# Kernel tuning notes

Hardware: AMD Instinct MI355X
Metric: run time of the kernel (lower is better)

Reference implementation:

```python
import jax, jax.numpy as jnp
import numpy as np
from jax import lax
from jax.scipy.special import logsumexp

V, E, H, T = 30000, 512, 512, 76   # vocab, embed, hidden, num_tags
B, S = 256, 128
HD = H // 2                        # per-direction hidden


def setup_inputs() -> dict:
    key = jax.random.key(0)
    ks = jax.random.split(key, 18)
    n = lambda k, shp: jax.random.normal(k, shp, dtype=jnp.float32) * 0.05
    return {
        "input_ids": jax.random.randint(ks[0], (B, S), 0, V),
        "tag_ids":   jax.random.randint(ks[1], (B, S), 0, 74),
        "lengths":   jax.random.randint(ks[2], (B,), 1, S + 1),
        "embed_table": n(ks[3], (V, E)),
        "W_ih_f": n(ks[4], (4 * HD, E)),  "W_hh_f": n(ks[5], (4 * HD, HD)),
        "b_ih_f": n(ks[6], (4 * HD,)),    "b_hh_f": n(ks[7], (4 * HD,)),
        "W_ih_b": n(ks[8], (4 * HD, E)),  "W_hh_b": n(ks[9], (4 * HD, HD)),
        "b_ih_b": n(ks[10], (4 * HD,)),   "b_hh_b": n(ks[11], (4 * HD,)),
        "W_out": n(ks[12], (T, H)),       "b_out": n(ks[13], (T,)),
        "start_trans": n(ks[14], (T,)),   "end_trans": n(ks[15], (T,)),
        "trans": n(ks[16], (T, T)),
        "h0": jax.random.normal(ks[17], (2, B, HD), dtype=jnp.float32),
        "c0": jax.random.normal(jax.random.fold_in(key, 99), (2, B, HD), dtype=jnp.float32),
    }


def _run_lstm(x, h, c, Wih, Whh, b):
    # x: (S,B,E); PyTorch gate order i,f,g,o
    def step(carry, xt):
        h, c = carry
        z = xt @ Wih.T + h @ Whh.T + b
        i, f, g, o = jnp.split(z, 4, axis=-1)
        c = jax.nn.sigmoid(f) * c + jax.nn.sigmoid(i) * jnp.tanh(g)
        h = jax.nn.sigmoid(o) * jnp.tanh(c)
        return (h, c), h
    _, hs = lax.scan(step, (h, c), x)
    return hs  # (S,B,HD)


def _crf_nll(em, tags, mask, start_trans, end_trans, trans):
    # em: (S,B,T) emissions, tags: (S,B) int, mask: (S,B) bool, mask[0]=True
    nb = em.shape[1]
    bidx = jnp.arange(nb)
    # --- numerator: score of gold path ---
    score0 = start_trans[tags[0]] + em[0, bidx, tags[0]]
    def num_step(carry, inp):
        score, prev = carry
        em_t, tag_t, m_t = inp
        s = trans[prev, tag_t] + em_t[bidx, tag_t]
        score = score + jnp.where(m_t, s, jnp.zeros_like(s))
        prev = jnp.where(m_t, tag_t, prev)
        return (score, prev), None
    (score, last_tags), _ = lax.scan(num_step, (score0, tags[0]), (em[1:], tags[1:], mask[1:]))
    score = score + end_trans[last_tags]
    # --- denominator: log partition via forward algorithm ---
    alpha0 = start_trans[None, :] + em[0]  # (B,T)
    def den_step(alpha, inp):
        em_t, m_t = inp
        nxt = logsumexp(alpha[:, :, None] + trans[None, :, :] + em_t[:, None, :], axis=1)
        return jnp.where(m_t[:, None], nxt, alpha), None
    alpha, _ = lax.scan(den_step, alpha0, (em[1:], mask[1:]))
    logZ = logsumexp(alpha + end_trans[None, :], axis=1)
    return score - logZ  # (B,) log-likelihood


def reference(input_ids, tag_ids, lengths, embed_table,
              W_ih_f, W_hh_f, b_ih_f, b_hh_f,
              W_ih_b, W_hh_b, b_ih_b, b_hh_b,
              W_out, b_out, start_trans, end_trans, trans, h0, c0):
    s = input_ids.shape[1]
    mask = jnp.arange(s)[None, :] < lengths[:, None]   # (B,S) left-aligned, col 0 all True
    x = embed_table[input_ids].transpose(1, 0, 2)      # (S,B,E)
    hf = _run_lstm(x, h0[0], c0[0], W_ih_f, W_hh_f, b_ih_f + b_hh_f)
    hb = _run_lstm(x[::-1], h0[1], c0[1], W_ih_b, W_hh_b, b_ih_b + b_hh_b)[::-1]
    feats = jnp.concatenate([hf, hb], axis=-1)         # (S,B,H)
    em = feats @ W_out.T + b_out                       # (S,B,T)
    llh = _crf_nll(em, tag_ids.T, mask.T, start_trans, end_trans, trans)
    return -jnp.mean(llh)                              # reduction='mean', negated
```

## Files before the change

kernel.cpp:

```cpp
#include <hip/hip_runtime.h>
#include <hip/hip_bf16.h>
#include <math.h>

namespace {

constexpr int cE  = 512;
constexpr int cH  = 512;
constexpr int cT  = 76;
constexpr int cB  = 256;
constexpr int cS  = 128;
constexpr int cHD = 256;
constexpr int cNG = 1024;
constexpr int cM  = cS * cB;
constexpr int cV  = 30000;
constexpr int cBH = cB * cHD;

typedef __attribute__((ext_vector_type(8))) short bf16x8;
typedef __attribute__((ext_vector_type(4))) float f32x4;
typedef unsigned long long ull_t;

typedef const __attribute__((address_space(1))) unsigned int* gas_ptr;
typedef __attribute__((address_space(3))) unsigned int* las_ptr;

__device__ __forceinline__ float fsig(float x) { return 1.0f / (1.0f + __expf(-x)); }
__device__ __forceinline__ float ftanh_(float x) {
  float e = __expf(2.0f * fabsf(x));
  float t = 1.0f - 2.0f / (e + 1.0f);
  return copysignf(t, x);
}
__device__ __forceinline__ unsigned short f2bf(float f) {
  __hip_bfloat16 h = __float2bfloat16(f);
  return *reinterpret_cast<unsigned short*>(&h);
}
__device__ __forceinline__ float bf2f(unsigned short u) {
  unsigned int v = ((unsigned int)u) << 16;
  return *reinterpret_cast<float*>(&v);
}
__device__ __forceinline__ void gload_lds16(const void* g, void* l) {
  __builtin_amdgcn_global_load_lds((gas_ptr)g, (las_ptr)l, 16, 0, 0);
}

__global__ __launch_bounds__(256) void k_prep(
    const float* __restrict__ embed,
    const float* __restrict__ Wihf, const float* __restrict__ Wihb,
    const float* __restrict__ Whhf, const float* __restrict__ Whhb,
    const float* __restrict__ h0,   const float* __restrict__ Wout,
    unsigned short* __restrict__ tbl, unsigned short* __restrict__ wih,
    unsigned short* __restrict__ whh, unsigned short* __restrict__ hInit,
    unsigned short* __restrict__ WoutP, unsigned int* __restrict__ bar)
{
  const int gid = blockIdx.x * 256 + threadIdx.x;
  if (gid < 512) bar[gid] = 0;
  constexpr int NT  = cV * cE / 4;
  constexpr int NI  = cNG * cE / 4;
  constexpr int NH  = cNG * cHD / 4;
  constexpr int NH0 = 2 * cBH / 4;
  constexpr int NW  = 128 * cE / 4;
  constexpr int total = NT + 2*NI + 2*NH + NH0 + NW;
  for (int q = gid; q < total; q += 4096 * 256) {
    const float* src; unsigned short* dst; int lq;
    bool zero = false;
    if (q < NT)               { src = embed; dst = tbl;              lq = q; }
    else if (q < NT+NI)       { src = Wihf;  dst = wih;              lq = q-NT; }
    else if (q < NT+2*NI)     { src = Wihb;  dst = wih + cNG*cE;     lq = q-NT-NI; }
    else if (q < NT+2*NI+NH)  { src = Whhf;  dst = whh;              lq = q-NT-2*NI; }
    else if (q < NT+2*NI+2*NH){ src = Whhb;  dst = whh + cNG*cHD;    lq = q-NT-2*NI-NH; }
    else if (q < NT+2*NI+2*NH+NH0){ src = h0; dst = hInit;           lq = q-NT-2*NI-2*NH; }
    else { lq = q-NT-2*NI-2*NH-NH0; src = Wout; dst = WoutP; zero = (lq >= cT*cE/4); }
    float4 v = make_float4(0.f,0.f,0.f,0.f);
    if (!zero) v = *(const float4*)(src + (size_t)lq * 4);
    ushort4 u;
    u.x = f2bf(v.x); u.y = f2bf(v.y); u.z = f2bf(v.z); u.w = f2bf(v.w);
    *(ushort4*)(dst + (size_t)lq * 4) = u;
  }
}

__global__ __launch_bounds__(256) void k_embed_mfma(
    const int* __restrict__ ids,
    const unsigned short* __restrict__ tbl,
    const unsigned short* __restrict__ Wih,
    const float* __restrict__ b1f, const float* __restrict__ b2f,
    const float* __restrict__ b1b, const float* __restrict__ b2b,
    __hip_bfloat16* __restrict__ Pf, __hip_bfloat16* __restrict__ Pb)
{
  const int bid = blockIdx.x;
  const int xcd = bid & 7;
  const int jj  = bid >> 3;
  const int m_tile = xcd * 32 + (jj >> 4);
  const int nz  = jj & 15;
  const int n_tile = nz & 7;
  const int d   = nz >> 3;

  const unsigned short* W = Wih + (size_t)d * cNG * cE;
  const float* b1 = d ? b1b : b1f;
  const float* b2 = d ? b2b : b2f;
  unsigned short* P = (unsigned short*)(d ? Pb : Pf);

  const int n0 = n_tile * 128;
  const int m0 = m_tile * 128;
  const int tid = threadIdx.x;

  __shared__ unsigned short Al[128 * 64];
  __shared__ unsigned short Bl[128 * 64];
  __shared__ float bias_s[128];
  if (tid < 128) bias_s[tid] = b1[n0 + tid] + b2[n0 + tid];

  const int lane = tid & 63, wave = tid >> 6;
  const int wm = wave >> 1, wn = wave & 1;
  const int fr = lane & 15, fq = lane >> 4;

  const int srow = wave * 32;
  const int lrow = lane >> 3;
  const int lch  = lane & 7;
  int aid[4];
#pragma unroll
  for (int q = 0; q < 4; ++q) {
    const int m = m0 + srow + q * 8 + lrow;
    aid[q] = ids[(m & (cB - 1)) * cS + (m >> 8)];
  }

  f32x4 acc[4][4];
#pragma unroll
  for (int i = 0; i < 4; ++i)
#pragma unroll
    for (int j = 0; j < 4; ++j) acc[i][j] = (f32x4){0.f, 0.f, 0.f, 0.f};

  for (int kt = 0; kt < cE / 64; ++kt) {
    __syncthreads();
#pragma unroll
    for (int q = 0; q < 4; ++q) {
      const unsigned short* ga = tbl + (size_t)aid[q] * cE + kt * 64 + lch * 8;
      const unsigned short* gb = W + (size_t)(n0 + srow + q * 8 + lrow) * cE + kt * 64 + lch * 8;
      gload_lds16(ga, Al + (srow + q * 8) * 64);
      gload_lds16(gb, Bl + (srow + q * 8) * 64);
    }
    __syncthreads();
#pragma unroll
    for (int ks = 0; ks < 2; ++ks) {
      bf16x8 aF[4], bF[4];
#pragma unroll
      for (int i = 0; i < 4; ++i)
        aF[i] = *(const bf16x8*)(Al + (wm * 64 + i * 16 + fr) * 64 + ks * 32 + fq * 8);
#pragma unroll
      for (int j = 0; j < 4; ++j)
        bF[j] = *(const bf16x8*)(Bl + (wn * 64 + j * 16 + fr) * 64 + ks * 32 + fq * 8);
#pragma unroll
      for (int i = 0; i < 4; ++i)
#pragma unroll
        for (int j = 0; j < 4; ++j)
          acc[i][j] = __builtin_amdgcn_mfma_f32_16x16x32_bf16(aF[i], bF[j], acc[i][j], 0, 0, 0);
    }
  }

#pragma unroll
  for (int i = 0; i < 4; ++i)
#pragma unroll
    for (int j = 0; j < 4; ++j) {
      const int gcol = wn * 64 + j * 16 + fr;
#pragma unroll
      for (int r = 0; r < 4; ++r) {
        const int grow = m0 + wm * 64 + i * 16 + fq * 4 + r;
        P[(size_t)grow * cNG + n0 + gcol] = f2bf(acc[i][j][r] + bias_s[gcol]);
      }
    }
}

__global__ __launch_bounds__(64, 1) void k_lstm_all(
    const unsigned short* __restrict__ Wbf,
    const unsigned short* __restrict__ Pf_,
    const unsigned short* __restrict__ Pb_,
    const float* __restrict__ c0,
    const unsigned short* __restrict__ hInit,
    ull_t* __restrict__ hHist,
    unsigned int* __restrict__ bar)
{
  const int bid = blockIdx.x;
  const int g   = bid & 15;
  const int m_  = bid >> 4;
  const int d   = g >> 3;
  const int b0  = (g & 7) * 32;
  const int j0  = m_ * 16;
  const int lane = threadIdx.x;
  const int fr = lane & 15, fq = lane >> 4;
  const int jj = j0 + fr;
  unsigned int* cnt = bar + g * 32;

  const unsigned short* P = d ? Pb_ : Pf_;
  const unsigned short* wbase = Wbf + (size_t)d * cNG * cHD;

  bf16x8 wreg[8][4];
#pragma unroll
  for (int k0 = 0; k0 < 8; ++k0)
#pragma unroll
    for (int gg = 0; gg < 4; ++gg)
      wreg[k0][gg] = *(const bf16x8*)(wbase + (size_t)(gg * cHD + j0 + fr) * cHD + k0 * 32 + fq * 8);

  float creg[8];
#pragma unroll
  for (int mf = 0; mf < 2; ++mf)
#pragma unroll
    for (int r = 0; r < 4; ++r)
      creg[mf * 4 + r] = c0[d * cBH + (b0 + mf * 16 + fq * 4 + r) * cHD + jj];

  __shared__ unsigned short hs[32 * 16];

  for (int t = 0; t < cS; ++t) {
    const int te = d ? (cS - 1 - t) : t;

    const ull_t* hsrc;
    if (t == 0) {
      hsrc = (const ull_t*)hInit + ((size_t)d * cBH >> 2);
    } else {
      const int tp = d ? (te + 1) : (te - 1);
      hsrc = hHist + ((((size_t)tp * 2 + d) * cBH) >> 2);
    }
    bf16x8 areg[2][8];
#pragma unroll
    for (int mf = 0; mf < 2; ++mf)
#pragma unroll
      for (int k0 = 0; k0 < 8; ++k0) {
        const size_t base = (((size_t)(b0 + mf * 16 + fr) * cHD + k0 * 32 + fq * 8) >> 2);
        union { ull_t u[2]; bf16x8 v; } tmp;
        tmp.u[0] = __hip_atomic_load((ull_t*)(hsrc + base),     __ATOMIC_RELAXED, __HIP_MEMORY_SCOPE_AGENT);
        tmp.u[1] = __hip_atomic_load((ull_t*)(hsrc + base + 1), __ATOMIC_RELAXED, __HIP_MEMORY_SCOPE_AGENT);
        areg[mf][k0] = tmp.v;
      }

    unsigned short pv[4][8];
    const unsigned short* Pt = P + (size_t)te * cB * cNG;
#pragma unroll
    for (int gg = 0; gg < 4; ++gg)
#pragma unroll
      for (int mf = 0; mf < 2; ++mf)
#pragma unroll
        for (int r = 0; r < 4; ++r)
          pv[gg][mf * 4 + r] = Pt[(size_t)(b0 + mf * 16 + fq * 4 + r) * cNG + gg * cHD + jj];

    f32x4 acc[2][4];
#pragma unroll
    for (int mf = 0; mf < 2; ++mf)
#pragma unroll
      for (int gg = 0; gg < 4; ++gg) acc[mf][gg] = (f32x4){0.f, 0.f, 0.f, 0.f};
#pragma unroll
    for (int k0 = 0; k0 < 8; ++k0)
#pragma unroll
      for (int gg = 0; gg < 4; ++gg) {
        acc[0][gg] = __builtin_amdgcn_mfma_f32_16x16x32_bf16(areg[0][k0], wreg[k0][gg], acc[0][gg], 0, 0, 0);
        acc[1][gg] = __builtin_amdgcn_mfma_f32_16x16x32_bf16(areg[1][k0], wreg[k0][gg], acc[1][gg], 0, 0, 0);
      }

#pragma unroll
    for (int mf = 0; mf < 2; ++mf)
#pragma unroll
      for (int r = 0; r < 4; ++r) {
        const float zi = acc[mf][0][r] + bf2f(pv[0][mf * 4 + r]);
        const float zf = acc[mf][1][r] + bf2f(pv[1][mf * 4 + r]);
        const float zg = acc[mf][2][r] + bf2f(pv[2][mf * 4 + r]);
        const float zo = acc[mf][3][r] + bf2f(pv[3][mf * 4 + r]);
        const float cc = fsig(zf) * creg[mf * 4 + r] + fsig(zi) * ftanh_(zg);
        creg[mf * 4 + r] = cc;
        hs[(mf * 16 + fq * 4 + r) * 16 + fr] = f2bf(fsig(zo) * ftanh_(cc));
      }

    {
      const int row = lane >> 1, half = lane & 1;
      const ull_t v0 = *(const ull_t*)(hs + row * 16 + half * 8);
      const ull_t v1 = *(const ull_t*)(hs + row * 16 + half * 8 + 4);
      const size_t idx = ((((size_t)te * 2 + d) * cBH) + (b0 + row) * cHD + j0 + half * 8) >> 2;
      __hip_atomic_store(hHist + idx,     v0, __ATOMIC_RELAXED, __HIP_MEMORY_SCOPE_AGENT);
      __hip_atomic_store(hHist + idx + 1, v1, __ATOMIC_RELAXED, __HIP_MEMORY_SCOPE_AGENT);
    }

    if (t != cS - 1) {
      __threadfence_block();
      if (lane == 0) {
        __hip_atomic_fetch_add(cnt, 1u, __ATOMIC_RELAXED, __HIP_MEMORY_SCOPE_AGENT);
        const unsigned int target = 16u * (unsigned int)(t + 1);
        while (__hip_atomic_load(cnt, __ATOMIC_RELAXED, __HIP_MEMORY_SCOPE_AGENT) < target)
          __builtin_amdgcn_s_sleep(1);
      }
      __threadfence_block();
    }
  }
}

__global__ __launch_bounds__(256) void k_em_mfma(
    const unsigned short* __restrict__ hHist,
    const unsigned short* __restrict__ WoutP,
    const float* __restrict__ b_out, float* __restrict__ em)
{
  const int m0 = blockIdx.x * 128;
  const int tid = threadIdx.x;

  __shared__ unsigned short Al[128 * 64];
  __shared__ unsigned short Bl[128 * 64];
  __shared__ float bias_s[128];
  if (tid < 128) bias_s[tid] = (tid < cT) ? b_out[tid] : 0.f;

  const int lane = tid & 63, wave = tid >> 6;
  const int wm = wave >> 1, wn = wave & 1;
  const int fr = lane & 15, fq = lane >> 4;
  const int srow = wave * 32;
  const int lrow = lane >> 3;
  const int lch  = lane & 7;

  f32x4 acc[4][4];
#pragma unroll
  for (int i = 0; i < 4; ++i)
#pragma unroll
    for (int j = 0; j < 4; ++j) acc[i][j] = (f32x4){0.f, 0.f, 0.f, 0.f};

  for (int kt = 0; kt < 8; ++kt) {
    const int d  = kt >> 2;
    const int ko = (kt & 3) * 64;
    __syncthreads();
#pragma unroll
    for (int q = 0; q < 4; ++q) {
      const int row = srow + q * 8 + lrow;
      const int m = m0 + row;
      const int t = m >> 8, b = m & 255;
      const unsigned short* ga = hHist + (((size_t)t * 2 + d) * cB + b) * cHD + ko + lch * 8;
      const unsigned short* gb = WoutP + (size_t)row * cH + kt * 64 + lch * 8;
      gload_lds16(ga, Al + (srow + q * 8) * 64);
      gload_lds16(gb, Bl + (srow + q * 8) * 64);
    }
    __syncthreads();
#pragma unroll
    for (int ks = 0; ks < 2; ++ks) {
      bf16x8 aF[4], bF[4];
#pragma unroll
      for (int i = 0; i < 4; ++i)
        aF[i] = *(const bf16x8*)(Al + (wm * 64 + i * 16 + fr) * 64 + ks * 32 + fq * 8);
#pragma unroll
      for (int j = 0; j < 4; ++j)
        bF[j] = *(const bf16x8*)(Bl + (wn * 64 + j * 16 + fr) * 64 + ks * 32 + fq * 8);
#pragma unroll
      for (int i = 0; i < 4; ++i)
#pragma unroll
        for (int j = 0; j < 4; ++j)
          acc[i][j] = __builtin_amdgcn_mfma_f32_16x16x32_bf16(aF[i], bF[j], acc[i][j], 0, 0, 0);
    }
  }

#pragma unroll
  for (int i = 0; i < 4; ++i)
#pragma unroll
    for (int j = 0; j < 4; ++j) {
      const int gcol = wn * 64 + j * 16 + fr;
      if (gcol < cT) {
#pragma unroll
        for (int r = 0; r < 4; ++r) {
          const int grow = m0 + wm * 64 + i * 16 + fq * 4 + r;
          em[(size_t)grow * cT + gcol] = acc[i][j][r] + bias_s[gcol];
        }
      }
    }
}

__global__ __launch_bounds__(320) void k_crf(
    const float* __restrict__ em,
    const int* __restrict__ tag_ids,
    const int* __restrict__ lengths,
    const float* __restrict__ start_trans,
    const float* __restrict__ end_trans,
    const float* __restrict__ trans,
    float* __restrict__ llh)
{
  const int b = blockIdx.x;
  const int tid = threadIdx.x;
  const int len = lengths[b];

  __shared__ float trans_t[80 * 81];
  __shared__ float em_s[cS * 80];
  __shared__ float a0[80], a1[80];
  __shared__ float red[128];
  __shared__ float score_sh;

  for (int idx = tid; idx < cT * cT; idx += 320) {
    const int i = idx / cT, jt = idx - i * cT;
    trans_t[jt * 81 + i] = trans[idx];
  }
  for (int idx = tid; idx < cS * cT; idx += 320) {
    const int t = idx / cT, jt = idx - t * cT;
    em_s[t * 80 + jt] = em[((size_t)t * cB + b) * cT + jt];
  }
  __syncthreads();

  float contrib = 0.f;
  if (tid < cS) {
    const int t = tid;
    if (t == 0) {
      const int tg = tag_ids[b * cS];
      contrib = start_trans[tg] + em_s[tg];
    } else if (t < len) {
      const int tg = tag_ids[b * cS + t];
      const int tp = tag_ids[b * cS + t - 1];
      contrib = trans_t[tg * 81 + tp] + em_s[t * 80 + tg];
    }
    if (t == len - 1) contrib += end_trans[tag_ids[b * cS + len - 1]];
  }
  if (tid < 128) red[tid] = contrib;
  __syncthreads();
  for (int s = 64; s > 0; s >>= 1) {
    if (tid < s) red[tid] += red[tid + s];
    __syncthreads();
  }
  if (tid == 0) score_sh = red[0];

  const int j   = tid >> 2;
  const int sub = tid & 3;
  const int i0  = sub * 19;
  float* cur = a0;
  float* nxt = a1;
  if (sub == 0 && j < cT) cur[j] = start_trans[j] + em_s[j];
  __syncthreads();
  for (int t = 1; t < len; ++t) {
    const float mref = cur[0];
    const float* trow = &trans_t[j * 81 + i0];
    const float* crow = &cur[i0];
    float s = 0.f;
#pragma unroll
    for (int q = 0; q < 19; ++q)
      s += __expf(crow[q] + trow[q] - mref);
    s += __shfl_xor(s, 1);
    s += __shfl_xor(s, 2);
    if (sub == 0 && j < cT) nxt[j] = mref + __logf(s) + em_s[t * 80 + j];
    __syncthreads();
    float* tp2 = cur; cur = nxt; nxt = tp2;
  }

  const float v = (tid < cT) ? cur[tid] + end_trans[tid] : -1e30f;
  if (tid < 128) red[tid] = v;
  __syncthreads();
  for (int s = 64; s > 0; s >>= 1) {
    if (tid < s) red[tid] = fmaxf(red[tid], red[tid + s]);
    __syncthreads();
  }
  const float mx = red[0];
  __syncthreads();
  if (tid < 128) red[tid] = (tid < cT) ? __expf(v - mx) : 0.f;
  __syncthreads();
  for (int s = 64; s > 0; s >>= 1) {
    if (tid < s) red[tid] += red[tid + s];
    __syncthreads();
  }
  if (tid == 0) llh[b] = score_sh - (mx + __logf(red[0]));
}

__global__ __launch_bounds__(256) void k_final(const float* __restrict__ llh,
                                               float* __restrict__ out)
{
  __shared__ float red[256];
  const int tid = threadIdx.x;
  red[tid] = llh[tid];
  __syncthreads();
  for (int s = 128; s > 0; s >>= 1) {
    if (tid < s) red[tid] += red[tid + s];
    __syncthreads();
  }
  if (tid == 0) out[0] = -red[0] * (1.0f / cB);
}

}

extern "C" void kernel_launch(void* const* d_in, const int* in_sizes, int n_in,
                              void* d_out, int out_size, void* d_ws, size_t ws_size,
                              hipStream_t stream) {
  const int*   input_ids   = (const int*)  d_in[0];
  const int*   tag_ids     = (const int*)  d_in[1];
  const int*   lengths     = (const int*)  d_in[2];
  const float* embed_table = (const float*)d_in[3];
  const float* W_ih_f      = (const float*)d_in[4];
  const float* W_hh_f      = (const float*)d_in[5];
  const float* b_ih_f      = (const float*)d_in[6];
  const float* b_hh_f      = (const float*)d_in[7];
  const float* W_ih_b      = (const float*)d_in[8];
  const float* W_hh_b      = (const float*)d_in[9];
  const float* b_ih_b      = (const float*)d_in[10];
  const float* b_hh_b      = (const float*)d_in[11];
  const float* W_out       = (const float*)d_in[12];
  const float* b_out       = (const float*)d_in[13];
  const float* start_trans = (const float*)d_in[14];
  const float* end_trans   = (const float*)d_in[15];
  const float* trans       = (const float*)d_in[16];
  const float* h0          = (const float*)d_in[17];
  const float* c0          = (const float*)d_in[18];
  float* out = (float*)d_out;

  char* wsb = (char*)d_ws;
  const size_t MB = 1024 * 1024;
  __hip_bfloat16* Pf = (__hip_bfloat16*)(wsb);
  __hip_bfloat16* Pb = (__hip_bfloat16*)(wsb + 64 * MB);
  unsigned short* tbl   = (unsigned short*)(wsb + 128 * MB);
  ull_t*          hHist = (ull_t*)         (wsb + 128 * MB);
  unsigned short* wih   = (unsigned short*)(wsb + 160 * MB);
  float*          em    = (float*)         (wsb + 165 * MB);
  unsigned short* whh   = (unsigned short*)(wsb + 176 * MB);
  unsigned short* hInit = (unsigned short*)(wsb + 177 * MB);
  unsigned short* WoutP = (unsigned short*)(wsb + 178 * MB);
  float*          llh   = (float*)         (wsb + 179 * MB);
  unsigned int*   bar   = (unsigned int*)  (wsb + 179 * MB + 4096);

  k_prep<<<4096, 256, 0, stream>>>(embed_table, W_ih_f, W_ih_b, W_hh_f, W_hh_b,
                                   h0, W_out, tbl, wih, whh, hInit, WoutP, bar);

  k_embed_mfma<<<4096, 256, 0, stream>>>(input_ids, tbl, wih,
                                         b_ih_f, b_hh_f, b_ih_b, b_hh_b, Pf, Pb);

  k_lstm_all<<<256, 64, 0, stream>>>(whh, (const unsigned short*)Pf,
                                     (const unsigned short*)Pb,
                                     c0, hInit, hHist, bar);

  k_em_mfma<<<cM / 128, 256, 0, stream>>>((const unsigned short*)hHist, WoutP,
                                          b_out, em);

  k_crf<<<cB, 320, 0, stream>>>(em, tag_ids, lengths, start_trans, end_trans, trans, llh);
  k_final<<<1, 256, 0, stream>>>(llh, out);
}
```

Measured before the change: 823.3 us.

## Replace cross-block atomic barrier LSTM with per-block batch-partitioned recurrence

The recurrent LSTM kernel drops its 256 single-wave blocks, which synchronised every step through global atomic counters and read h from global memory. It now runs 32 blocks of 1024 threads, each owning 16 batch rows for one direction, and keeps the hidden state in a double-buffered LDS tile synchronised with __syncthreads. Next-step input projections are prefetched during the MFMA work. This removes the global-memory spin barrier and h round-trip per step, at the cost of using only 32 CUs with 16 waves each holding large register weight tiles.

```diff
diff --git a/kernel.cpp b/kernel.cpp
--- a/kernel.cpp
+++ b/kernel.cpp
@@ -47,10 +47,9 @@
     const float* __restrict__ h0,   const float* __restrict__ Wout,
     unsigned short* __restrict__ tbl, unsigned short* __restrict__ wih,
     unsigned short* __restrict__ whh, unsigned short* __restrict__ hInit,
-    unsigned short* __restrict__ WoutP, unsigned int* __restrict__ bar)
+    unsigned short* __restrict__ WoutP)
 {
   const int gid = blockIdx.x * 256 + threadIdx.x;
-  if (gid < 512) bar[gid] = 0;
   constexpr int NT  = cV * cE / 4;
   constexpr int NI  = cNG * cE / 4;
   constexpr int NH  = cNG * cHD / 4;
@@ -165,29 +164,29 @@
     }
 }
 
-__global__ __launch_bounds__(64, 1) void k_lstm_all(
+__global__ __launch_bounds__(1024, 4) void k_lstm_block(
     const unsigned short* __restrict__ Wbf,
     const unsigned short* __restrict__ Pf_,
     const unsigned short* __restrict__ Pb_,
     const float* __restrict__ c0,
     const unsigned short* __restrict__ hInit,
-    ull_t* __restrict__ hHist,
-    unsigned int* __restrict__ bar)
+    unsigned short* __restrict__ hHist)
 {
   const int bid = blockIdx.x;
-  const int g   = bid & 15;
-  const int m_  = bid >> 4;
-  const int d   = g >> 3;
-  const int b0  = (g & 7) * 32;
-  const int j0  = m_ * 16;
-  const int lane = threadIdx.x;
+  const int d   = bid & 1;
+  const int b0  = (bid >> 1) * 16;
+  const int tid = threadIdx.x;
+  const int lane = tid & 63, w = tid >> 6;
   const int fr = lane & 15, fq = lane >> 4;
+  const int j0 = w * 16;
   const int jj = j0 + fr;
-  unsigned int* cnt = bar + g * 32;
 
   const unsigned short* P = d ? Pb_ : Pf_;
   const unsigned short* wbase = Wbf + (size_t)d * cNG * cHD;
 
+  constexpr int RS = 264;
+  __shared__ unsigned short Abuf[2][16 * RS];
+
   bf16x8 wreg[8][4];
 #pragma unroll
   for (int k0 = 0; k0 < 8; ++k0)
@@ -195,92 +194,78 @@
     for (int gg = 0; gg < 4; ++gg)
       wreg[k0][gg] = *(const bf16x8*)(wbase + (size_t)(gg * cHD + j0 + fr) * cHD + k0 * 32 + fq * 8);
 
-  float creg[8];
-#pragma unroll
-  for (int mf = 0; mf < 2; ++mf)
-#pragma unroll
-    for (int r = 0; r < 4; ++r)
-      creg[mf * 4 + r] = c0[d * cBH + (b0 + mf * 16 + fq * 4 + r) * cHD + jj];
-
-  __shared__ unsigned short hs[32 * 16];
+  float creg[4];
+#pragma unroll
+  for (int r = 0; r < 4; ++r)
+    creg[r] = c0[d * cBH + (b0 + fq * 4 + r) * cHD + jj];
+
+  {
+    const int row = tid >> 6;
+    const int c4  = (tid & 63) * 4;
+    const ushort4 v = *(const ushort4*)(hInit + (size_t)d * cBH + (b0 + row) * cHD + c4);
+    *(ushort4*)(&Abuf[0][row * RS + c4]) = v;
+  }
+
+  unsigned short pv[4][4], pvn[4][4];
+  {
+    const unsigned short* Pt = P + (size_t)(d ? cS - 1 : 0) * cB * cNG;
+#pragma unroll
+    for (int gg = 0; gg < 4; ++gg)
+#pragma unroll
+      for (int r = 0; r < 4; ++r)
+        pv[gg][r] = Pt[(size_t)(b0 + fq * 4 + r) * cNG + gg * cHD + jj];
+  }
+  __syncthreads();
 
   for (int t = 0; t < cS; ++t) {
     const int te = d ? (cS - 1 - t) : t;
-
-    const ull_t* hsrc;
-    if (t == 0) {
-      hsrc = (const ull_t*)hInit + ((size_t)d * cBH >> 2);
-    } else {
-      const int tp = d ? (te + 1) : (te - 1);
-      hsrc = hHist + ((((size_t)tp * 2 + d) * cBH) >> 2);
-    }
-    bf16x8 areg[2][8];
-#pragma unroll
-    for (int mf = 0; mf < 2; ++mf)
-#pragma unroll
-      for (int k0 = 0; k0 < 8; ++k0) {
-        const size_t base = (((size_t)(b0 + mf * 16 + fr) * cHD + k0 * 32 + fq * 8) >> 2);
-        union { ull_t u[2]; bf16x8 v; } tmp;
-        tmp.u[0] = __hip_atomic_load((ull_t*)(hsrc + base),     __ATOMIC_RELAXED, __HIP_MEMORY_SCOPE_AGENT);
-        tmp.u[1] = __hip_atomic_load((ull_t*)(hsrc + base + 1), __ATOMIC_RELAXED, __HIP_MEMORY_SCOPE_AGENT);
-        areg[mf][k0] = tmp.v;
-      }
-
-    unsigned short pv[4][8];
-    const unsigned short* Pt = P + (size_t)te * cB * cNG;
+    const unsigned short* cur = Abuf[t & 1];
+    unsigned short* nxt = Abuf[(t + 1) & 1];
+
+    bf16x8 aF[8];
+#pragma unroll
+    for (int k0 = 0; k0 < 8; ++k0)
+      aF[k0] = *(const bf16x8*)(cur + fr * RS + k0 * 32 + fq * 8);
+
+    f32x4 acc[4];
+#pragma unroll
+    for (int gg = 0; gg < 4; ++gg) acc[gg] = (f32x4){0.f, 0.f, 0.f, 0.f};
+#pragma unroll
+    for (int k0 = 0; k0 < 8; ++k0)
+#pragma unroll
+      for (int gg = 0; gg < 4; ++gg)
+        acc[gg] = __builtin_amdgcn_mfma_f32_16x16x32_bf16(aF[k0], wreg[k0][gg], acc[gg], 0, 0, 0);
+
+    if (t != cS - 1) {
+      const int tn = d ? (te - 1) : (te + 1);
+      const unsigned short* Pt = P + (size_t)tn * cB * cNG;
+#pragma unroll
+      for (int gg = 0; gg < 4; ++gg)
+#pragma unroll
+        for (int r = 0; r < 4; ++r)
+          pvn[gg][r] = Pt[(size_t)(b0 + fq * 4 + r) * cNG + gg * cHD + jj];
+    }
+
+#pragma unroll
+    for (int r = 0; r < 4; ++r) {
+      const int row = fq * 4 + r;
+      const float zi = acc[0][r] + bf2f(pv[0][r]);
+      const float zf = acc[1][r] + bf2f(pv[1][r]);
+      const float zg = acc[2][r] + bf2f(pv[2][r]);
+      const float zo = acc[3][r] + bf2f(pv[3][r]);
+      const float cc = fsig(zf) * creg[r] + fsig(zi) * ftanh_(zg);
+      creg[r] = cc;
+      const unsigned short h = f2bf(fsig(zo) * ftanh_(cc));
+      nxt[row * RS + jj] = h;
+      hHist[(((size_t)te * 2 + d) * cB + b0 + row) * cHD + jj] = h;
+    }
+
 #pragma unroll
     for (int gg = 0; gg < 4; ++gg)
 #pragma unroll
-      for (int mf = 0; mf < 2; ++mf)
-#pragma unroll
-        for (int r = 0; r < 4; ++r)
-          pv[gg][mf * 4 + r] = Pt[(size_t)(b0 + mf * 16 + fq * 4 + r) * cNG + gg * cHD + jj];
-
-    f32x4 acc[2][4];
-#pragma unroll
-    for (int mf = 0; mf < 2; ++mf)
-#pragma unroll
-      for (int gg = 0; gg < 4; ++gg) acc[mf][gg] = (f32x4){0.f, 0.f, 0.f, 0.f};
-#pragma unroll
-    for (int k0 = 0; k0 < 8; ++k0)
-#pragma unroll
-      for (int gg = 0; gg < 4; ++gg) {
-        acc[0][gg] = __builtin_amdgcn_mfma_f32_16x16x32_bf16(areg[0][k0], wreg[k0][gg], acc[0][gg], 0, 0, 0);
-        acc[1][gg] = __builtin_amdgcn_mfma_f32_16x16x32_bf16(areg[1][k0], wreg[k0][gg], acc[1][gg], 0, 0, 0);
-      }
-
-#pragma unroll
-    for (int mf = 0; mf < 2; ++mf)
-#pragma unroll
-      for (int r = 0; r < 4; ++r) {
-        const float zi = acc[mf][0][r] + bf2f(pv[0][mf * 4 + r]);
-        const float zf = acc[mf][1][r] + bf2f(pv[1][mf * 4 + r]);
-        const float zg = acc[mf][2][r] + bf2f(pv[2][mf * 4 + r]);
-        const float zo = acc[mf][3][r] + bf2f(pv[3][mf * 4 + r]);
-        const float cc = fsig(zf) * creg[mf * 4 + r] + fsig(zi) * ftanh_(zg);
-        creg[mf * 4 + r] = cc;
-        hs[(mf * 16 + fq * 4 + r) * 16 + fr] = f2bf(fsig(zo) * ftanh_(cc));
-      }
-
-    {
-      const int row = lane >> 1, half = lane & 1;
-      const ull_t v0 = *(const ull_t*)(hs + row * 16 + half * 8);
-      const ull_t v1 = *(const ull_t*)(hs + row * 16 + half * 8 + 4);
-      const size_t idx = ((((size_t)te * 2 + d) * cBH) + (b0 + row) * cHD + j0 + half * 8) >> 2;
-      __hip_atomic_store(hHist + idx,     v0, __ATOMIC_RELAXED, __HIP_MEMORY_SCOPE_AGENT);
-      __hip_atomic_store(hHist + idx + 1, v1, __ATOMIC_RELAXED, __HIP_MEMORY_SCOPE_AGENT);
-    }
-
-    if (t != cS - 1) {
-      __threadfence_block();
-      if (lane == 0) {
-        __hip_atomic_fetch_add(cnt, 1u, __ATOMIC_RELAXED, __HIP_MEMORY_SCOPE_AGENT);
-        const unsigned int target = 16u * (unsigned int)(t + 1);
-        while (__hip_atomic_load(cnt, __ATOMIC_RELAXED, __HIP_MEMORY_SCOPE_AGENT) < target)
-          __builtin_amdgcn_s_sleep(1);
-      }
-      __threadfence_block();
-    }
+      for (int r = 0; r < 4; ++r) pv[gg][r] = pvn[gg][r];
+
+    __syncthreads();
   }
 }
 
@@ -492,27 +477,25 @@
   __hip_bfloat16* Pf = (__hip_bfloat16*)(wsb);
   __hip_bfloat16* Pb = (__hip_bfloat16*)(wsb + 64 * MB);
   unsigned short* tbl   = (unsigned short*)(wsb + 128 * MB);
-  ull_t*          hHist = (ull_t*)         (wsb + 128 * MB);
+  unsigned short* hHist = (unsigned short*)(wsb + 128 * MB);
   unsigned short* wih   = (unsigned short*)(wsb + 160 * MB);
   float*          em    = (float*)         (wsb + 165 * MB);
   unsigned short* whh   = (unsigned short*)(wsb + 176 * MB);
   unsigned short* hInit = (unsigned short*)(wsb + 177 * MB);
   unsigned short* WoutP = (unsigned short*)(wsb + 178 * MB);
   float*          llh   = (float*)         (wsb + 179 * MB);
-  unsigned int*   bar   = (unsigned int*)  (wsb + 179 * MB + 4096);
 
   k_prep<<<4096, 256, 0, stream>>>(embed_table, W_ih_f, W_ih_b, W_hh_f, W_hh_b,
-                                   h0, W_out, tbl, wih, whh, hInit, WoutP, bar);
+                                   h0, W_out, tbl, wih, whh, hInit, WoutP);
 
   k_embed_mfma<<<4096, 256, 0, stream>>>(input_ids, tbl, wih,
                                          b_ih_f, b_hh_f, b_ih_b, b_hh_b, Pf, Pb);
 
-  k_lstm_all<<<256, 64, 0, stream>>>(whh, (const unsigned short*)Pf,
-                                     (const unsigned short*)Pb,
-                                     c0, hInit, hHist, bar);
-
-  k_em_mfma<<<cM / 128, 256, 0, stream>>>((const unsigned short*)hHist, WoutP,
-                                          b_out, em);
+  k_lstm_block<<<32, 1024, 0, stream>>>(whh, (const unsigned short*)Pf,
+                                        (const unsigned short*)Pb,
+                                        c0, hInit, hHist);
+
+  k_em_mfma<<<cM / 128, 256, 0, stream>>>(hHist, WoutP, b_out, em);
 
   k_crf<<<cB, 320, 0, stream>>>(em, tag_ids, lengths, start_trans, end_trans, trans, llh);
   k_final<<<1, 256, 0, stream>>>(llh, out);
```

After: 1.719 ms. 109% more time.

## Group four LSTM waves per block and prefetch next-step gate inputs

Applied to the files above, without the earlier changes.

The recurrent LSTM kernel goes from 256 single-wave blocks to 64 blocks of four waves. Each block covers 64 hidden units of one batch group, so each cross-block barrier has 4 participants instead of 16, using __syncthreads within the block and a spin with s_sleep(0). The precomputed input projection for the next timestep is now loaded before the barrier wait, hiding that global load latency behind synchronisation. The trade-off is intra-block syncs and more registers per thread, on fewer CUs.

```diff
diff --git a/kernel.cpp b/kernel.cpp
--- a/kernel.cpp
+++ b/kernel.cpp
@@ -50,7 +50,7 @@
     unsigned short* __restrict__ WoutP, unsigned int* __restrict__ bar)
 {
   const int gid = blockIdx.x * 256 + threadIdx.x;
-  if (gid < 512) bar[gid] = 0;
+  if (gid < 1024) bar[gid] = 0;
   constexpr int NT  = cV * cE / 4;
   constexpr int NI  = cNG * cE / 4;
   constexpr int NH  = cNG * cHD / 4;
@@ -165,26 +165,29 @@
     }
 }
 
-__global__ __launch_bounds__(64, 1) void k_lstm_all(
+__global__ __launch_bounds__(256, 1) void k_lstm_grp(
     const unsigned short* __restrict__ Wbf,
     const unsigned short* __restrict__ Pf_,
     const unsigned short* __restrict__ Pb_,
     const float* __restrict__ c0,
     const unsigned short* __restrict__ hInit,
-    ull_t* __restrict__ hHist,
+    unsigned short* __restrict__ hHist,
     unsigned int* __restrict__ bar)
 {
   const int bid = blockIdx.x;
-  const int g   = bid & 15;
-  const int m_  = bid >> 4;
+  const int g   = bid >> 2;
+  const int mem = bid & 3;
   const int d   = g >> 3;
   const int b0  = (g & 7) * 32;
-  const int j0  = m_ * 16;
-  const int lane = threadIdx.x;
+  const int tid = threadIdx.x;
+  const int lane = tid & 63, w = tid >> 6;
   const int fr = lane & 15, fq = lane >> 4;
+  const int j0 = (mem * 4 + w) * 16;
   const int jj = j0 + fr;
   unsigned int* cnt = bar + g * 32;
 
+  __shared__ unsigned short hs[4][512];
+
   const unsigned short* P = d ? Pb_ : Pf_;
   const unsigned short* wbase = Wbf + (size_t)d * cNG * cHD;
 
@@ -202,39 +205,38 @@
     for (int r = 0; r < 4; ++r)
       creg[mf * 4 + r] = c0[d * cBH + (b0 + mf * 16 + fq * 4 + r) * cHD + jj];
 
-  __shared__ unsigned short hs[32 * 16];
+  unsigned short pv[4][8], pvn[4][8];
+  {
+    const unsigned short* Pt = P + (size_t)(d ? cS - 1 : 0) * cB * cNG;
+#pragma unroll
+    for (int gg = 0; gg < 4; ++gg)
+#pragma unroll
+      for (int mf = 0; mf < 2; ++mf)
+#pragma unroll
+        for (int r = 0; r < 4; ++r)
+          pv[gg][mf * 4 + r] = Pt[(size_t)(b0 + mf * 16 + fq * 4 + r) * cNG + gg * cHD + jj];
+  }
 
   for (int t = 0; t < cS; ++t) {
     const int te = d ? (cS - 1 - t) : t;
 
-    const ull_t* hsrc;
-    if (t == 0) {
-      hsrc = (const ull_t*)hInit + ((size_t)d * cBH >> 2);
-    } else {
+    const unsigned short* hsrc;
+    if (t == 0) hsrc = hInit + (size_t)d * cBH;
+    else {
       const int tp = d ? (te + 1) : (te - 1);
-      hsrc = hHist + ((((size_t)tp * 2 + d) * cBH) >> 2);
+      hsrc = hHist + (((size_t)tp * 2 + d) * cBH);
     }
     bf16x8 areg[2][8];
 #pragma unroll
     for (int mf = 0; mf < 2; ++mf)
 #pragma unroll
       for (int k0 = 0; k0 < 8; ++k0) {
-        const size_t base = (((size_t)(b0 + mf * 16 + fr) * cHD + k0 * 32 + fq * 8) >> 2);
+        const ull_t* ap = (const ull_t*)(hsrc + (size_t)(b0 + mf * 16 + fr) * cHD + k0 * 32 + fq * 8);
         union { ull_t u[2]; bf16x8 v; } tmp;
-        tmp.u[0] = __hip_atomic_load((ull_t*)(hsrc + base),     __ATOMIC_RELAXED, __HIP_MEMORY_SCOPE_AGENT);
-        tmp.u[1] = __hip_atomic_load((ull_t*)(hsrc + base + 1), __ATOMIC_RELAXED, __HIP_MEMORY_SCOPE_AGENT);
+        tmp.u[0] = __hip_atomic_load((ull_t*)ap,       __ATOMIC_RELAXED, __HIP_MEMORY_SCOPE_AGENT);
+        tmp.u[1] = __hip_atomic_load((ull_t*)(ap + 1), __ATOMIC_RELAXED, __HIP_MEMORY_SCOPE_AGENT);
         areg[mf][k0] = tmp.v;
       }
-
-    unsigned short pv[4][8];
-    const unsigned short* Pt = P + (size_t)te * cB * cNG;
-#pragma unroll
-    for (int gg = 0; gg < 4; ++gg)
-#pragma unroll
-      for (int mf = 0; mf < 2; ++mf)
-#pragma unroll
-        for (int r = 0; r < 4; ++r)
-          pv[gg][mf * 4 + r] = Pt[(size_t)(b0 + mf * 16 + fq * 4 + r) * cNG + gg * cHD + jj];
 
     f32x4 acc[2][4];
 #pragma unroll
@@ -259,27 +261,43 @@
         const float zo = acc[mf][3][r] + bf2f(pv[3][mf * 4 + r]);
         const float cc = fsig(zf) * creg[mf * 4 + r] + fsig(zi) * ftanh_(zg);
         creg[mf * 4 + r] = cc;
-        hs[(mf * 16 + fq * 4 + r) * 16 + fr] = f2bf(fsig(zo) * ftanh_(cc));
+        hs[w][(mf * 16 + fq * 4 + r) * 16 + fr] = f2bf(fsig(zo) * ftanh_(cc));
       }
+    __syncthreads();
 
     {
       const int row = lane >> 1, half = lane & 1;
-      const ull_t v0 = *(const ull_t*)(hs + row * 16 + half * 8);
-      const ull_t v1 = *(const ull_t*)(hs + row * 16 + half * 8 + 4);
-      const size_t idx = ((((size_t)te * 2 + d) * cBH) + (b0 + row) * cHD + j0 + half * 8) >> 2;
-      __hip_atomic_store(hHist + idx,     v0, __ATOMIC_RELAXED, __HIP_MEMORY_SCOPE_AGENT);
-      __hip_atomic_store(hHist + idx + 1, v1, __ATOMIC_RELAXED, __HIP_MEMORY_SCOPE_AGENT);
+      const size_t idx = (((size_t)te * 2 + d) * cBH) + (size_t)(b0 + row) * cHD + j0 + half * 8;
+      __hip_atomic_store((ull_t*)(hHist + idx),     *(const ull_t*)(&hs[w][row * 16 + half * 8]),
+                         __ATOMIC_RELAXED, __HIP_MEMORY_SCOPE_AGENT);
+      __hip_atomic_store((ull_t*)(hHist + idx + 4), *(const ull_t*)(&hs[w][row * 16 + half * 8 + 4]),
+                         __ATOMIC_RELAXED, __HIP_MEMORY_SCOPE_AGENT);
     }
 
     if (t != cS - 1) {
-      __threadfence_block();
-      if (lane == 0) {
+      const int tn = d ? (te - 1) : (te + 1);
+      const unsigned short* Pt = P + (size_t)tn * cB * cNG;
+#pragma unroll
+      for (int gg = 0; gg < 4; ++gg)
+#pragma unroll
+        for (int mf = 0; mf < 2; ++mf)
+#pragma unroll
+          for (int r = 0; r < 4; ++r)
+            pvn[gg][mf * 4 + r] = Pt[(size_t)(b0 + mf * 16 + fq * 4 + r) * cNG + gg * cHD + jj];
+
+      __syncthreads();
+      if (tid == 0) {
+        const unsigned int target = 4u * (unsigned int)(t + 1);
         __hip_atomic_fetch_add(cnt, 1u, __ATOMIC_RELAXED, __HIP_MEMORY_SCOPE_AGENT);
-        const unsigned int target = 16u * (unsigned int)(t + 1);
         while (__hip_atomic_load(cnt, __ATOMIC_RELAXED, __HIP_MEMORY_SCOPE_AGENT) < target)
-          __builtin_amdgcn_s_sleep(1);
+          __builtin_amdgcn_s_sleep(0);
       }
-      __threadfence_block();
+      __syncthreads();
+
+#pragma unroll
+      for (int gg = 0; gg < 4; ++gg)
+#pragma unroll
+        for (int q = 0; q < 8; ++q) pv[gg][q] = pvn[gg][q];
     }
   }
 }
@@ -492,7 +510,7 @@
   __hip_bfloat16* Pf = (__hip_bfloat16*)(wsb);
   __hip_bfloat16* Pb = (__hip_bfloat16*)(wsb + 64 * MB);
   unsigned short* tbl   = (unsigned short*)(wsb + 128 * MB);
-  ull_t*          hHist = (ull_t*)         (wsb + 128 * MB);
+  unsigned short* hHist = (unsigned short*)(wsb + 128 * MB);
   unsigned short* wih   = (unsigned short*)(wsb + 160 * MB);
   float*          em    = (float*)         (wsb + 165 * MB);
   unsigned short* whh   = (unsigned short*)(wsb + 176 * MB);
@@ -507,12 +525,11 @@
   k_embed_mfma<<<4096, 256, 0, stream>>>(input_ids, tbl, wih,
                                          b_ih_f, b_hh_f, b_ih_b, b_hh_b, Pf, Pb);
 
-  k_lstm_all<<<256, 64, 0, stream>>>(whh, (const unsigned short*)Pf,
+  k_lstm_grp<<<64, 256, 0, stream>>>(whh, (const unsigned short*)Pf,
                                      (const unsigned short*)Pb,
                                      c0, hInit, hHist, bar);
 
-  k_em_mfma<<<cM / 128, 256, 0, stream>>>((const unsigned short*)hHist, WoutP,
-                                          b_out, em);
+  k_em_mfma<<<cM / 128, 256, 0, stream>>>(hHist, WoutP, b_out, em);
 
   k_crf<<<cB, 320, 0, stream>>>(em, tag_ids, lengths, start_trans, end_trans, trans, llh);
   k_final<<<1, 256, 0, stream>>>(llh, out);
```

New measurement: 1.093 ms. 32.8% more time.
